# Performance work log

Measured on AMD Instinct MI355X. Metric: run time of the kernel, lower is better.

Reference implementation:

```python
import jax, jax.numpy as jnp
import numpy as np
import math

S, B, H, NH, HD = 2048, 1, 4096, 32, 128
ROT = HD // 2  # 2D RoPE: each half of head_dim gets its own rotary embedding


def _rotate_half(x):
    x1, x2 = jnp.split(x, 2, axis=-1)
    return jnp.concatenate((-x2, x1), axis=-1)


def _rope_tables(max_pos, dim):
    inv_freq = 1.0 / (10000.0 ** (jnp.arange(0, dim, 2, dtype=jnp.float32) / dim))
    freqs = jnp.arange(max_pos, dtype=jnp.float32)[:, None] * inv_freq[None, :]  # [P, dim/2]
    emb = jnp.concatenate((freqs, freqs), axis=-1)  # [P, dim]
    return jnp.cos(emb), jnp.sin(emb)


def _apply_rope(q, k, cos_t, sin_t, pid):
    # q,k: [S,B,NH,ROT]; pid: [S,B]
    c = cos_t[pid][:, :, None, :]  # [S,B,1,ROT]
    s = sin_t[pid][:, :, None, :]
    return q * c + _rotate_half(q) * s, k * c + _rotate_half(k) * s


def setup_inputs() -> dict:
    key = jax.random.key(0)
    k1, k2, k3, k4, k5 = jax.random.split(key, 5)
    hidden_states = jax.random.normal(k1, (S, B, H), dtype=jnp.float32)
    pos = jnp.arange(S, dtype=jnp.int32)[None, :]          # [1,S] standard positions
    blk = jnp.zeros((1, S), dtype=jnp.int32)                # block positions (pre-gmask all zeros)
    position_ids = jnp.stack([pos, blk], axis=1)            # [B,2,S]
    # causal mask: True = masked out
    attention_mask = jnp.triu(jnp.ones((S, S), dtype=bool), k=1)[None, None]  # [B,1,S,S]
    Wqkv = jax.random.normal(k2, (3 * H, H), dtype=jnp.float32) * 0.02
    bqkv = jax.random.normal(k3, (3 * H,), dtype=jnp.float32) * 0.02
    Wd = jax.random.normal(k4, (H, H), dtype=jnp.float32) * 0.02
    bd = jax.random.normal(k5, (H,), dtype=jnp.float32) * 0.02
    return {"hidden_states": hidden_states, "position_ids": position_ids,
            "attention_mask": attention_mask, "layer_id": 5,
            "Wqkv": Wqkv, "bqkv": bqkv, "Wd": Wd, "bd": bd}


def reference(hidden_states, position_ids, attention_mask, layer_id, Wqkv, bqkv, Wd, bd):
    # QKV projection: [S,B,H] -> [S,B,NH,3*HD]
    mixed = hidden_states @ Wqkv.T + bqkv
    mixed = mixed.reshape(S, B, NH, 3 * HD)
    q, k, v = jnp.split(mixed, 3, axis=-1)  # each [S,B,NH,HD]

    # 2D rotary position embedding on the two head-dim halves
    q1, q2 = jnp.split(q, 2, axis=-1)
    k1, k2 = jnp.split(k, 2, axis=-1)
    cos_t, sin_t = _rope_tables(S, ROT)
    pid = position_ids[:, 0, :].T   # [S,B]
    bid = position_ids[:, 1, :].T   # [S,B]
    q1, k1 = _apply_rope(q1, k1, cos_t, sin_t, pid)
    q2, k2 = _apply_rope(q2, k2, cos_t, sin_t, bid)
    q = jnp.concatenate([q1, q2], axis=-1)
    k = jnp.concatenate([k1, k2], axis=-1)

    # layer-scaled attention scores
    coeff = float(layer_id + 1)
    q = q / (math.sqrt(HD) * coeff)
    scores = jnp.einsum('sbnd,tbnd->bnst', q, k)  # [B,NH,S,S]
    scores = jnp.where(attention_mask, jnp.float32(-10000.0), scores)
    scores = scores.astype(jnp.float32) * coeff
    probs = jax.nn.softmax(scores, axis=-1).astype(hidden_states.dtype)

    ctx = jnp.einsum('bnst,tbnd->sbnd', probs, v).reshape(S, B, NH * HD)
    return ctx @ Wd.T + bd  # [S,B,H]
```

## Files before the change

### kernel.cpp

```cpp
#include <hip/hip_runtime.h>


#define S_LEN 2048
#define NHEAD 32
#define HDIM 128
#define HID 4096

typedef float f32x4 __attribute__((ext_vector_type(4)));
typedef __bf16 bf16x8 __attribute__((ext_vector_type(8)));
typedef __bf16 bf16x4 __attribute__((ext_vector_type(4)));
typedef _Float16 f16x4 __attribute__((ext_vector_type(4)));
typedef _Float16 f16x8 __attribute__((ext_vector_type(8)));

__device__ __forceinline__ void gload16(const void* g, void* l) {
  __builtin_amdgcn_global_load_lds(
      (const __attribute__((address_space(1))) void*)g,
      (__attribute__((address_space(3))) void*)l, 16, 0, 0);
}

__global__ __launch_bounds__(256) void cvt_f32_bf16_kernel(
    const float* __restrict__ in, __bf16* __restrict__ out, int n4) {
  int i = blockIdx.x * 256 + threadIdx.x;
  if (i >= n4) return;
  f32x4 v = *(const f32x4*)(in + (size_t)i * 4);
  bf16x4 o;
  o[0] = (__bf16)v[0]; o[1] = (__bf16)v[1];
  o[2] = (__bf16)v[2]; o[3] = (__bf16)v[3];
  *(bf16x4*)(out + (size_t)i * 4) = o;
}

__device__ __forceinline__ void stage_half(const __bf16* __restrict__ G,
                                           int grow0, int Kstride, int kofs,
                                           __bf16* lds_half, int tid) {
#pragma unroll
  for (int i = 0; i < 2; ++i) {
    int idx = i * 512 + tid;
    int rr = idx >> 3;
    int offp = (idx & 7) * 16;
    int off = offp ^ ((rr & 7) << 4);
    const char* src =
        (const char*)(G + (size_t)(grow0 + rr) * Kstride + kofs) + off;
    char* dst = (char*)lds_half + idx * 16;
    gload16(src, dst);
  }
}

__device__ __forceinline__ bf16x8 ldsfrag(const __bf16* hb, int rowin, int ks,
                                          int lg) {
  int off = ((ks * 64 + lg * 16) ^ ((rowin & 7) << 4));
  return *(const bf16x8*)((const char*)hb + rowin * 128 + off);
}

#define READ_A(DST, SLOT)                                                     \
  _Pragma("unroll") for (int mi = 0; mi < 4; ++mi)                            \
      _Pragma("unroll") for (int ks = 0; ks < 2; ++ks) DST[mi][ks] =          \
      ldsfrag(SLOT, wm * 64 + mi * 16 + lr, ks, lg);

#define READ_B(DST, SLOT)                                                     \
  _Pragma("unroll") for (int nj = 0; nj < 2; ++nj)                            \
      _Pragma("unroll") for (int ks = 0; ks < 2; ++ks) DST[nj][ks] =          \
      ldsfrag(SLOT, wn * 32 + nj * 16 + lr, ks, lg);

#define MFMA_Q(MH, NH, AFR, BFR)                                              \
  __builtin_amdgcn_s_setprio(1);                                              \
  _Pragma("unroll") for (int mi = 0; mi < 4; ++mi)                            \
      _Pragma("unroll") for (int nj = 0; nj < 2; ++nj)                        \
          _Pragma("unroll") for (int ks = 0; ks < 2; ++ks)                    \
              acc[MH][NH][mi][nj] =                                           \
      __builtin_amdgcn_mfma_f32_16x16x32_bf16(AFR[mi][ks], BFR[nj][ks],       \
                                              acc[MH][NH][mi][nj], 0, 0, 0);  \
  __builtin_amdgcn_s_setprio(0);

#define BAR asm volatile("s_barrier" ::: "memory");

template <int OUT_MODE>
__global__ __launch_bounds__(512, 2) void gemm256_kernel(
    const __bf16* __restrict__ A, const __bf16* __restrict__ B,
    const float* __restrict__ bias, void* __restrict__ Cout, int M, int N,
    int Kstride, int klen, int mtiles, int ksplit) {
  __shared__ __align__(16) __bf16 As[2][2][128 * 64];
  __shared__ __align__(16) __bf16 Bs[2][2][128 * 64];
  const int tid = threadIdx.x;
  int bid = blockIdx.x;
  int kh = 0;
  if (ksplit == 2) { kh = bid & 1; bid >>= 1; }
  const int kbase = kh * klen;
  int per_patch = mtiles * 8;
  int p = bid / per_patch, r = bid % per_patch;
  int mt = r % mtiles, nt = p * 8 + r / mtiles;
  int m0 = mt * 256, n0 = nt * 256;
  const int wid = tid >> 6, l = tid & 63;
  const int wm = wid >> 2, wn = wid & 3;
  const int lr = l & 15, lg = l >> 4;
  const int nk = klen >> 6;

  f32x4 acc[2][2][4][2];
#pragma unroll
  for (int a = 0; a < 2; ++a)
#pragma unroll
    for (int b = 0; b < 2; ++b)
#pragma unroll
      for (int c = 0; c < 4; ++c)
#pragma unroll
        for (int d = 0; d < 2; ++d) acc[a][b][c][d] = 0.f;

  stage_half(A, m0, Kstride, kbase, &As[0][0][0], tid);
  stage_half(B, n0, Kstride, kbase, &Bs[0][0][0], tid);
  stage_half(B, n0 + 128, Kstride, kbase, &Bs[0][1][0], tid);
  stage_half(A, m0 + 128, Kstride, kbase, &As[0][1][0], tid);
  stage_half(A, m0, Kstride, kbase + 64, &As[1][0][0], tid);
  stage_half(B, n0, Kstride, kbase + 64, &Bs[1][0][0], tid);
  stage_half(B, n0 + 128, Kstride, kbase + 64, &Bs[1][1][0], tid);
  stage_half(A, m0 + 128, Kstride, kbase + 64, &As[1][1][0], tid);
  asm volatile("s_waitcnt vmcnt(8)" ::: "memory");
  BAR;

  for (int t = 0; t < nk; ++t) {
    const int cur = t & 1;
    const __bf16* A0s = &As[cur][0][0];
    const __bf16* A1s = &As[cur][1][0];
    const __bf16* B0s = &Bs[cur][0][0];
    const __bf16* B1s = &Bs[cur][1][0];
    const int kt2 = kbase + (t + 2) * 64;
    const bool s2 = (t + 2 < nk);

    bf16x8 a[4][2], b0[2][2], b1[2][2];
    READ_A(a, A0s);
    READ_B(b0, B0s);
    MFMA_Q(0, 0, a, b0);
    READ_B(b1, B1s);
    MFMA_Q(0, 1, a, b1);
    READ_A(a, A1s);
    MFMA_Q(1, 1, a, b1);
    BAR;
    if (s2) {
      stage_half(A, m0, Kstride, kt2, &As[cur][0][0], tid);
      stage_half(B, n0, Kstride, kt2, &Bs[cur][0][0], tid);
      stage_half(B, n0 + 128, Kstride, kt2, &Bs[cur][1][0], tid);
      stage_half(A, m0 + 128, Kstride, kt2, &As[cur][1][0], tid);
    }
    MFMA_Q(1, 0, a, b0);
    if (s2)
      asm volatile("s_waitcnt vmcnt(8)" ::: "memory");
    else
      asm volatile("s_waitcnt vmcnt(0)" ::: "memory");
    BAR;
  }

  float* outF = (float*)Cout;
  if (OUT_MODE == 2) outF += (size_t)kh * M * N;
#pragma unroll
  for (int mh = 0; mh < 2; ++mh)
#pragma unroll
    for (int nh = 0; nh < 2; ++nh)
#pragma unroll
      for (int mi = 0; mi < 4; ++mi)
#pragma unroll
        for (int nj = 0; nj < 2; ++nj) {
          int row = m0 + mh * 128 + wm * 64 + mi * 16 + lg * 4;
          int col = n0 + nh * 128 + wn * 32 + nj * 16 + lr;
          float bv = (OUT_MODE == 2) ? 0.f : bias[col];
          f32x4 v = acc[mh][nh][mi][nj];
#pragma unroll
          for (int j = 0; j < 4; ++j) {
            float o = v[j] + bv;
            if (OUT_MODE == 1)
              ((__bf16*)Cout)[(size_t)(row + j) * N + col] = (__bf16)o;
            else
              outF[(size_t)(row + j) * N + col] = o;
          }
        }
}

__global__ __launch_bounds__(256) void reduce_addbias_kernel(
    const float* __restrict__ p0, const float* __restrict__ p1,
    const float* __restrict__ bias, float* __restrict__ out) {
  int i = blockIdx.x * 256 + threadIdx.x;
  int col = (i * 4) & (HID - 1);
  f32x4 a = *(const f32x4*)(p0 + (size_t)i * 4);
  f32x4 b = *(const f32x4*)(p1 + (size_t)i * 4);
  f32x4 c = *(const f32x4*)(bias + col);
  a = a + b + c;
  *(f32x4*)(out + (size_t)i * 4) = a;
}

__global__ __launch_bounds__(256) void rope_kernel(
    const __bf16* __restrict__ qkv, const int* __restrict__ pos_ids,
    __bf16* __restrict__ Q, __bf16* __restrict__ K, _Float16* __restrict__ VT) {
  int h = blockIdx.x & 31, sb = blockIdx.x >> 5;
  int s0 = sb * 64;
  int t = threadIdx.x;
  __shared__ float cs[64][2][2][32];
  __shared__ _Float16 vs[64][132];

  for (int idx = t; idx < 64 * 64; idx += 256) {
    int sl = idx >> 6, half = (idx >> 5) & 1, i = idx & 31;
    int p = pos_ids[half * S_LEN + s0 + sl];
    float f = powf(10000.f, -(float)i / 32.f);
    float ang = (float)p * f;
    cs[sl][half][0][i] = cosf(ang);
    cs[sl][half][1][i] = sinf(ang);
  }
#pragma unroll
  for (int c = 0; c < 4; c++) {
    int chunk = c * 256 + t;
    int slv = chunk >> 4, co = (chunk & 15) * 8;
    const __bf16* vsrc =
        qkv + (size_t)(s0 + slv) * (NHEAD * 3 * HDIM) + h * 384 + 256 + co;
    bf16x8 vv = *(const bf16x8*)vsrc;
    f16x4 a, b;
#pragma unroll
    for (int j = 0; j < 4; j++) {
      a[j] = (_Float16)(float)vv[j];
      b[j] = (_Float16)(float)vv[4 + j];
    }
    *(f16x4*)&vs[slv][co] = a;
    *(f16x4*)&vs[slv][co + 4] = b;
  }
  __syncthreads();

  {
    int sl = t >> 2, role = t & 3;
    int isK = role >> 1, half = role & 1;
    const __bf16* src = qkv + (size_t)(s0 + sl) * (NHEAD * 3 * HDIM) + h * 384 +
                        isK * 128 + half * 64;
    float scale = isK ? 1.f : 0.08838834764831845f;
    float x[64];
    bf16x8 buf[8];
#pragma unroll
    for (int c = 0; c < 8; c++) buf[c] = *(const bf16x8*)(src + c * 8);
#pragma unroll
    for (int c = 0; c < 8; c++)
#pragma unroll
      for (int j = 0; j < 8; j++) x[c * 8 + j] = (float)buf[c][j];
    bf16x8 ob[8];
#pragma unroll
    for (int i = 0; i < 64; i++) {
      int ii = i & 31;
      float cv = cs[sl][half][0][ii], sv = cs[sl][half][1][ii];
      float partner = (i < 32) ? x[i + 32] : x[i - 32];
      float sgn = (i < 32) ? -1.f : 1.f;
      float o = (x[i] * cv + sgn * partner * sv) * scale;
      ob[i >> 3][i & 7] = (__bf16)o;
    }
    __bf16* dst = (isK ? K : Q) + ((size_t)h * S_LEN + s0 + sl) * HDIM + half * 64;
#pragma unroll
    for (int c = 0; c < 8; c++) *(bf16x8*)(dst + c * 8) = ob[c];
  }

#pragma unroll
  for (int c = 0; c < 4; c++) {
    int chunk = c * 256 + t;
    int d = chunk >> 3, so = (chunk & 7) * 8;
    f16x8 o;
#pragma unroll
    for (int j = 0; j < 8; j++) o[j] = vs[so + j][d];
    *(f16x8*)(VT + ((size_t)h * HDIM + d) * S_LEN + s0 + so) = o;
  }
}

__global__ __launch_bounds__(256, 2) void attn_kernel(
    const __bf16* __restrict__ Q, const __bf16* __restrict__ K,
    const _Float16* __restrict__ VT, __bf16* __restrict__ ctx) {
  int b = blockIdx.x;
  int h = b & 31;
  int qb = 15 - (b >> 5);
  int w = threadIdx.x >> 6, l = threadIdx.x & 63;
  int lr = l & 15, lg = l >> 4;
  int q0 = qb * 128 + w * 32;
  const __bf16* Qh = Q + (size_t)h * S_LEN * HDIM;
  const __bf16* Kh = K + (size_t)h * S_LEN * HDIM;
  const _Float16* Vh = VT + (size_t)h * HDIM * S_LEN;

  bf16x8 qfA[4], qfB[4];
#pragma unroll
  for (int kk = 0; kk < 4; kk++) {
    qfA[kk] = *(const bf16x8*)(Qh + (size_t)(q0 + lr) * HDIM + kk * 32 + lg * 8);
    qfB[kk] =
        *(const bf16x8*)(Qh + (size_t)(q0 + 16 + lr) * HDIM + kk * 32 + lg * 8);
  }

  f32x4 accA[8], accB[8];
#pragma unroll
  for (int tt = 0; tt < 8; tt++) { accA[tt] = 0.f; accB[tt] = 0.f; }
  float mA = -INFINITY, lsA = 0.f, mB = -INFINITY, lsB = 0.f;
  int qgA = q0 + lr, qgB = q0 + 16 + lr;
  int qmax = q0 + 31;

  for (int kv0 = 0; kv0 <= qmax; kv0 += 16) {
    f32x4 stA = 0.f, stB = 0.f;
#pragma unroll
    for (int kk = 0; kk < 4; kk++) {
      bf16x8 kf =
          *(const bf16x8*)(Kh + (size_t)(kv0 + lr) * HDIM + kk * 32 + lg * 8);
      stA = __builtin_amdgcn_mfma_f32_16x16x32_bf16(kf, qfA[kk], stA, 0, 0, 0);
      stB = __builtin_amdgcn_mfma_f32_16x16x32_bf16(kf, qfB[kk], stB, 0, 0, 0);
    }
    float tmA = -INFINITY, tmB = -INFINITY;
#pragma unroll
    for (int j = 0; j < 4; j++) {
      int kvg = kv0 + lg * 4 + j;
      if (kvg > qgA) stA[j] = -INFINITY;
      if (kvg > qgB) stB[j] = -INFINITY;
      tmA = fmaxf(tmA, stA[j]);
      tmB = fmaxf(tmB, stB[j]);
    }
    tmA = fmaxf(tmA, __shfl_xor(tmA, 16));
    tmA = fmaxf(tmA, __shfl_xor(tmA, 32));
    tmB = fmaxf(tmB, __shfl_xor(tmB, 16));
    tmB = fmaxf(tmB, __shfl_xor(tmB, 32));
    int need = __any((tmA > mA) || (tmB > mB));
    float mnA = fmaxf(mA, tmA), mnB = fmaxf(mB, tmB);

    f16x4 paA, paB;
    float tsA = 0.f, tsB = 0.f;
#pragma unroll
    for (int j = 0; j < 4; j++) {
      float pA = __expf(stA[j] - mnA);
      float pB = __expf(stB[j] - mnB);
      tsA += pA; tsB += pB;
      paA[j] = (_Float16)pA; paB[j] = (_Float16)pB;
    }
    tsA += __shfl_xor(tsA, 16);
    tsA += __shfl_xor(tsA, 32);
    tsB += __shfl_xor(tsB, 16);
    tsB += __shfl_xor(tsB, 32);

    if (need) {
      float scA = __expf(mA - mnA), scB = __expf(mB - mnB);
      lsA = lsA * scA + tsA;
      lsB = lsB * scB + tsB;
      float sAj[4], sBj[4];
#pragma unroll
      for (int j = 0; j < 4; j++) {
        sAj[j] = __shfl(scA, lg * 4 + j);
        sBj[j] = __shfl(scB, lg * 4 + j);
      }
#pragma unroll
      for (int tt = 0; tt < 8; tt++)
#pragma unroll
        for (int j = 0; j < 4; j++) {
          accA[tt][j] *= sAj[j];
          accB[tt][j] *= sBj[j];
        }
    } else {
      lsA += tsA;
      lsB += tsB;
    }
    mA = mnA; mB = mnB;

#pragma unroll
    for (int tt = 0; tt < 8; tt++) {
      f16x4 vb =
          *(const f16x4*)(Vh + (size_t)(tt * 16 + lr) * S_LEN + kv0 + lg * 4);
      accA[tt] = __builtin_amdgcn_mfma_f32_16x16x16f16(paA, vb, accA[tt], 0, 0, 0);
      accB[tt] = __builtin_amdgcn_mfma_f32_16x16x16f16(paB, vb, accB[tt], 0, 0, 0);
    }
  }

  float rA[4], rB[4];
#pragma unroll
  for (int j = 0; j < 4; j++) {
    rA[j] = 1.f / __shfl(lsA, lg * 4 + j);
    rB[j] = 1.f / __shfl(lsB, lg * 4 + j);
  }
#pragma unroll
  for (int tt = 0; tt < 8; tt++) {
#pragma unroll
    for (int j = 0; j < 4; j++) {
      int qoA = q0 + lg * 4 + j;
      int qoB = q0 + 16 + lg * 4 + j;
      ctx[(size_t)qoA * (NHEAD * HDIM) + h * HDIM + tt * 16 + lr] =
          (__bf16)(accA[tt][j] * rA[j]);
      ctx[(size_t)qoB * (NHEAD * HDIM) + h * HDIM + tt * 16 + lr] =
          (__bf16)(accB[tt][j] * rB[j]);
    }
  }
}

extern "C" void kernel_launch(void* const* d_in, const int* in_sizes, int n_in,
                              void* d_out, int out_size, void* d_ws,
                              size_t ws_size, hipStream_t stream) {
  const float* hs = (const float*)d_in[0];
  const int* pos_ids = (const int*)d_in[1];
  const float* Wqkv = (const float*)d_in[4];
  const float* bqkv = (const float*)d_in[5];
  const float* Wd = (const float*)d_in[6];
  const float* bd = (const float*)d_in[7];
  float* out = (float*)d_out;

  char* ws = (char*)d_ws;
  constexpr size_t OFF_W = 16777216ULL;
  constexpr size_t OFF_QKV = OFF_W + 100663296ULL;
  constexpr size_t OFF_Q = OFF_QKV + 50331648ULL;
  constexpr size_t OFF_K = OFF_Q + 16777216ULL;
  constexpr size_t OFF_V = OFF_K + 16777216ULL;
  __bf16* hsb = (__bf16*)(ws);
  __bf16* wqkvb = (__bf16*)(ws + OFF_W);
  __bf16* wdb = (__bf16*)(ws + OFF_W);
  float* pk = (float*)(ws + OFF_W + 33554432ULL);
  __bf16* qkvb = (__bf16*)(ws + OFF_QKV);
  __bf16* ctxb = qkvb;
  __bf16* Qb = (__bf16*)(ws + OFF_Q);
  __bf16* Kb = (__bf16*)(ws + OFF_K);
  _Float16* Vtb = (_Float16*)(ws + OFF_V);

  cvt_f32_bf16_kernel<<<(S_LEN * HID) / 4 / 256, 256, 0, stream>>>(
      hs, hsb, S_LEN * HID / 4);
  cvt_f32_bf16_kernel<<<(3 * HID * HID) / 4 / 256, 256, 0, stream>>>(
      Wqkv, wqkvb, 3 * HID * HID / 4);

  gemm256_kernel<1><<<8 * 48, 512, 0, stream>>>(hsb, wqkvb, bqkv, qkvb, S_LEN,
                                                3 * HID, HID, HID, 8, 1);

  cvt_f32_bf16_kernel<<<(HID * HID) / 4 / 256, 256, 0, stream>>>(
      Wd, wdb, HID * HID / 4);

  rope_kernel<<<NHEAD * (S_LEN / 64), 256, 0, stream>>>(qkvb, pos_ids, Qb, Kb,
                                                        Vtb);

  attn_kernel<<<NHEAD * (S_LEN / 128), 256, 0, stream>>>(Qb, Kb, Vtb, ctxb);

  gemm256_kernel<2><<<2 * 8 * 16, 512, 0, stream>>>(ctxb, wdb, bd, pk, S_LEN,
                                                    HID, HID, HID / 2, 8, 2);
  reduce_addbias_kernel<<<(S_LEN * HID) / 4 / 256, 256, 0, stream>>>(
      pk, pk + (size_t)S_LEN * HID, bd, out);
}
```

Before: 696.8 us.

## Interleave per-quadrant LDS staging with MFMA phases in the 256x256 GEMM loop

Restructures the GEMM main loop into a ping-pong style schedule. Each quarter-tile LDS read is followed by issuing one half-tile global-to-LDS prefetch, then barriers and an lgkmcnt wait before the MFMA quadrant. The A1 half for the next step is loaded one iteration ahead, and the vmcnt waits are adjusted to match. The goal is to spread memory issue across the compute phases instead of bursting all four stages together. The cost is many more barriers per iteration.

```diff
diff --git a/kernel.cpp b/kernel.cpp
--- a/kernel.cpp
+++ b/kernel.cpp
@@ -72,6 +72,9 @@
   __builtin_amdgcn_s_setprio(0);
 
 #define BAR asm volatile("s_barrier" ::: "memory");
+#define LGKM0                                                                 \
+  asm volatile("s_waitcnt lgkmcnt(0)" ::: "memory");                          \
+  __builtin_amdgcn_sched_barrier(0);
 
 template <int OUT_MODE>
 __global__ __launch_bounds__(512, 2) void gemm256_kernel(
@@ -108,40 +111,50 @@
   stage_half(B, n0, Kstride, kbase, &Bs[0][0][0], tid);
   stage_half(B, n0 + 128, Kstride, kbase, &Bs[0][1][0], tid);
   stage_half(A, m0 + 128, Kstride, kbase, &As[0][1][0], tid);
-  stage_half(A, m0, Kstride, kbase + 64, &As[1][0][0], tid);
-  stage_half(B, n0, Kstride, kbase + 64, &Bs[1][0][0], tid);
-  stage_half(B, n0 + 128, Kstride, kbase + 64, &Bs[1][1][0], tid);
-  stage_half(A, m0 + 128, Kstride, kbase + 64, &As[1][1][0], tid);
-  asm volatile("s_waitcnt vmcnt(8)" ::: "memory");
+  if (nk > 1) {
+    stage_half(A, m0, Kstride, kbase + 64, &As[1][0][0], tid);
+    stage_half(B, n0, Kstride, kbase + 64, &Bs[1][0][0], tid);
+    stage_half(B, n0 + 128, Kstride, kbase + 64, &Bs[1][1][0], tid);
+    asm volatile("s_waitcnt vmcnt(6)" ::: "memory");
+  } else {
+    asm volatile("s_waitcnt vmcnt(0)" ::: "memory");
+  }
   BAR;
 
   for (int t = 0; t < nk; ++t) {
-    const int cur = t & 1;
-    const __bf16* A0s = &As[cur][0][0];
-    const __bf16* A1s = &As[cur][1][0];
-    const __bf16* B0s = &Bs[cur][0][0];
-    const __bf16* B1s = &Bs[cur][1][0];
+    const int cur = t & 1, nxt = cur ^ 1;
+    const int kt1 = kbase + (t + 1) * 64;
     const int kt2 = kbase + (t + 2) * 64;
-    const bool s2 = (t + 2 < nk);
-
+    const bool s1 = (t + 1 < nk), s2 = (t + 2 < nk);
     bf16x8 a[4][2], b0[2][2], b1[2][2];
-    READ_A(a, A0s);
-    READ_B(b0, B0s);
+
+    READ_A(a, &As[cur][0][0]);
+    READ_B(b0, &Bs[cur][0][0]);
+    if (s1) stage_half(A, m0 + 128, Kstride, kt1, &As[nxt][1][0], tid);
+    BAR;
+    LGKM0;
     MFMA_Q(0, 0, a, b0);
-    READ_B(b1, B1s);
+    BAR;
+
+    READ_B(b1, &Bs[cur][1][0]);
+    if (s2) stage_half(A, m0, Kstride, kt2, &As[cur][0][0], tid);
+    BAR;
+    LGKM0;
     MFMA_Q(0, 1, a, b1);
-    READ_A(a, A1s);
+    BAR;
+
+    READ_A(a, &As[cur][1][0]);
+    if (s2) stage_half(B, n0 + 128, Kstride, kt2, &Bs[cur][1][0], tid);
+    BAR;
+    LGKM0;
     MFMA_Q(1, 1, a, b1);
     BAR;
-    if (s2) {
-      stage_half(A, m0, Kstride, kt2, &As[cur][0][0], tid);
-      stage_half(B, n0, Kstride, kt2, &Bs[cur][0][0], tid);
-      stage_half(B, n0 + 128, Kstride, kt2, &Bs[cur][1][0], tid);
-      stage_half(A, m0 + 128, Kstride, kt2, &As[cur][1][0], tid);
-    }
+
+    if (s2) stage_half(B, n0, Kstride, kt2, &Bs[cur][0][0], tid);
+    BAR;
     MFMA_Q(1, 0, a, b0);
     if (s2)
-      asm volatile("s_waitcnt vmcnt(8)" ::: "memory");
+      asm volatile("s_waitcnt vmcnt(6)" ::: "memory");
     else
       asm volatile("s_waitcnt vmcnt(0)" ::: "memory");
     BAR;
```

Result: faster. 663.7 us (-4.8%).
